# Kernel optimization log

Measured on AMD Instinct MI355X. Metric: run time of the kernel, lower is better.

Reference implementation:

```python
import jax, jax.numpy as jnp
import numpy as np

B, L, ENC_IN, C_OUT = 8, 8192, 21, 21
D_MODEL, D_STATE, D_CONV, EXPAND = 512, 16, 4, 2
D_INNER = EXPAND * D_MODEL
DT_RANK = -(-D_MODEL // 16)  # 'auto' -> ceil(d_model/16) = 32
PRED_LEN = 720


def setup_inputs() -> dict:
    key = jax.random.key(0)
    ks = jax.random.split(key, 16)
    s = lambda k, sh, sc=0.02: jax.random.normal(k, sh, jnp.float32) * sc
    # Mamba-style dt bias init: dt ~ exp(U(log dt_min, log dt_max)), bias = softplus^{-1}(dt)
    dt = jnp.exp(jax.random.uniform(ks[9], (D_INNER,), jnp.float32,
                                    float(np.log(1e-3)), float(np.log(0.1))))
    b_dt = jnp.log(jnp.expm1(dt))
    return dict(
        x_enc=jax.random.normal(ks[0], (B, L, ENC_IN), jnp.float32),
        x_mark_enc=jax.random.normal(ks[1], (B, L, 4), jnp.float32),
        x_dec=jax.random.normal(ks[2], (B, PRED_LEN, ENC_IN), jnp.float32),
        x_mark_dec=jax.random.normal(ks[3], (B, PRED_LEN, 4), jnp.float32),
        W_embed=s(ks[4], (ENC_IN, D_MODEL)),
        b_embed=jnp.zeros((D_MODEL,), jnp.float32),
        W_in=s(ks[5], (D_MODEL, 2 * D_INNER)),
        conv_w=s(ks[6], (D_INNER, D_CONV), 0.1),
        conv_b=jnp.zeros((D_INNER,), jnp.float32),
        W_xproj=s(ks[7], (D_INNER, DT_RANK + 2 * D_STATE)),
        W_dt=s(ks[8], (DT_RANK, D_INNER), 0.1),
        b_dt=b_dt,
        A_log=jnp.log(jnp.tile(jnp.arange(1, D_STATE + 1, dtype=jnp.float32), (D_INNER, 1))),
        D=jnp.ones((D_INNER,), jnp.float32),
        W_out_ssm=s(ks[10], (D_INNER, D_MODEL)),
        W_proj=s(ks[11], (D_MODEL, C_OUT)),
        b_proj=jnp.zeros((C_OUT,), jnp.float32),
    )


def _mamba(x, W_in, conv_w, conv_b, W_xproj, W_dt, b_dt, A_log, D):
    b, l, _ = x.shape
    d_inner, d_conv = conv_w.shape
    d_state = A_log.shape[1]
    dt_rank = W_dt.shape[0]
    xz = x @ W_in                                   # [b,l,2*d_inner]
    u, z = jnp.split(xz, 2, axis=-1)
    # causal depthwise conv over time
    uc = jnp.transpose(u, (0, 2, 1))                # [b,d_inner,l]
    uc = jax.lax.conv_general_dilated(uc, conv_w[:, None, :], (1,),
                                      [(d_conv - 1, 0)],
                                      feature_group_count=d_inner)
    u = jax.nn.silu(jnp.transpose(uc, (0, 2, 1)) + conv_b)
    x_dbl = u @ W_xproj
    dt, Bm, Cm = jnp.split(x_dbl, [dt_rank, dt_rank + d_state], axis=-1)
    delta = jax.nn.softplus(dt @ W_dt + b_dt)       # [b,l,d_inner]
    A = -jnp.exp(A_log)                             # [d_inner,d_state]

    def step(h, inp):
        d_t, B_t, C_t, u_t = inp                    # [b,d_inner],[b,d_state],[b,d_state],[b,d_inner]
        dA = jnp.exp(d_t[..., None] * A)            # [b,d_inner,d_state]
        h = dA * h + (d_t * u_t)[..., None] * B_t[:, None, :]
        y = jnp.einsum('bds,bs->bd', h, C_t)
        return h, y

    h0 = jnp.zeros((b, d_inner, d_state), u.dtype)
    xs = (jnp.moveaxis(delta, 1, 0), jnp.moveaxis(Bm, 1, 0),
          jnp.moveaxis(Cm, 1, 0), jnp.moveaxis(u, 1, 0))
    _, ys = jax.lax.scan(step, h0, xs)              # ys: [l,b,d_inner]
    y = jnp.moveaxis(ys, 0, 1) + u * D
    return y * jax.nn.silu(z)


def reference(x_enc, x_mark_enc, x_dec, x_mark_dec, W_embed, b_embed, W_in,
              conv_w, conv_b, W_xproj, W_dt, b_dt, A_log, D, W_out_ssm,
              W_proj, b_proj):
    # RevIN normalize (stats detached, matching .detach() in torch)
    means = jax.lax.stop_gradient(x_enc.mean(axis=1, keepdims=True))
    xc = x_enc - means
    stdev = jax.lax.stop_gradient(jnp.sqrt(jnp.var(xc, axis=1, keepdims=True) + 1e-5))
    xn = xc / stdev
    emb = xn @ W_embed + b_embed                    # [b,L,d_model]
    y = _mamba(emb, W_in, conv_w, conv_b, W_xproj, W_dt, b_dt, A_log, D)
    y = y @ W_out_ssm                               # [b,L,d_model]
    y = y[:, -PRED_LEN:, :]                         # L >= pred_len branch
    out = y @ W_proj + b_proj                       # [b,pred_len,c_out]
    out = out * stdev[:, :1, :] + means[:, :1, :]   # RevIN denorm (c_out == enc_in)
    return out
```

## Files before the change

kernel.cpp:

```cpp
#include <hip/hip_runtime.h>
#include <hip/hip_bf16.h>
#include <stdint.h>

#define B_    8
#define L_    8192
#define CIN   21
#define DM    512
#define DI    1024
#define DS    16
#define DTR   32
#define PRED  720
#define L0    (L_ - PRED)
#define CHUNK 128
#define NCHK  64
#define NTCH  6
#define TAIL0 7424
#define NSUB  24
#define TROWS 768

#define UIDX(b, row, dblk, dl) ((((size_t)(b) * 16 + (dblk)) * L_ + (row)) * 64 + (dl))
#define TIDX(b, row, dblk, dl) ((((size_t)(b) * 16 + (dblk)) * TROWS + (row)) * 64 + (dl))
#define QIDX(b, c, dblk, s, dl) \
  ((((((size_t)(b) * NCHK + (c)) * 16 + (dblk)) * 16 + (s)) * 64) + (dl))
#define SIDX(b, si, dblk, s, dl) \
  ((((((size_t)(b) * NSUB + (si)) * 16 + (dblk)) * 16 + (s)) * 64) + (dl))

typedef __bf16 bf16_t;
typedef __attribute__((ext_vector_type(4))) __bf16 bf16x4;
typedef __attribute__((ext_vector_type(8))) __bf16 bf16x8;
typedef __attribute__((ext_vector_type(4))) float f32x4;
typedef __attribute__((ext_vector_type(2))) float f32x2;

__device__ __forceinline__ void gl_lds16(const void* g, void* l) {
  __builtin_amdgcn_global_load_lds(
      (const __attribute__((address_space(1))) unsigned int*)g,
      (__attribute__((address_space(3))) unsigned int*)l, 16, 0, 0);
}

__device__ __forceinline__ float b2f(bf16_t v) { return (float)v; }
__device__ __forceinline__ bf16_t f2b(float v) { return (bf16_t)v; }

__global__ void zero_kernel(float* __restrict__ out, int n) {
  int i = blockIdx.x * 256 + threadIdx.x;
  if (i < n) out[i] = 0.f;
}

__global__ __launch_bounds__(256) void stats_kernel(const float* __restrict__ x,
                                                    float* __restrict__ stats) {
  const int b = blockIdx.x / CIN, c = blockIdx.x % CIN;
  const int tid = threadIdx.x;
  float s = 0.f, s2 = 0.f;
  for (int l = tid; l < L_; l += 256) {
    float v = x[((size_t)b * L_ + l) * CIN + c];
    s += v; s2 += v * v;
  }
  __shared__ float rs[256], rs2[256];
  rs[tid] = s; rs2[tid] = s2;
  __syncthreads();
  for (int o = 128; o > 0; o >>= 1) {
    if (tid < o) { rs[tid] += rs[tid + o]; rs2[tid] += rs2[tid + o]; }
    __syncthreads();
  }
  if (tid == 0) {
    float mean = rs[0] / (float)L_;
    float var  = rs2[0] / (float)L_ - mean * mean;
    stats[(b * CIN + c) * 2]     = mean;
    stats[(b * CIN + c) * 2 + 1] = sqrtf(var + 1e-5f);
  }
}

__global__ void tconv_kernel(const float* __restrict__ in, bf16_t* __restrict__ out,
                             int R, int C) {
  int idx = blockIdx.x * 256 + threadIdx.x;
  if (idx < R * C) {
    int r = idx / C, c = idx % C;
    out[(size_t)c * R + r] = f2b(in[idx]);
  }
}
__global__ void tconvf_kernel(const float* __restrict__ in, float* __restrict__ out,
                              int R, int C) {
  int idx = blockIdx.x * 256 + threadIdx.x;
  if (idx < R * C) {
    int r = idx / C, c = idx % C;
    out[(size_t)c * R + r] = in[idx];
  }
}

__global__ __launch_bounds__(256) void wcomb_kernel(const float* __restrict__ We,
                                                    const float* __restrict__ be,
                                                    const float* __restrict__ Win,
                                                    float* __restrict__ Wcu,
                                                    float* __restrict__ Wcz) {
  int idx = blockIdx.x * 256 + threadIdx.x;
  if (idx >= 22 * 2048) return;
  int c = idx / 2048, n = idx % 2048;
  float a = 0.f;
  if (c < 21) {
    for (int k = 0; k < DM; ++k) a = fmaf(We[c * DM + k], Win[(size_t)k * 2048 + n], a);
  } else {
    for (int k = 0; k < DM; ++k) a = fmaf(be[k], Win[(size_t)k * 2048 + n], a);
  }
  if (n < DI) Wcu[c * DI + n] = a;
  else        Wcz[c * DI + (n - DI)] = a;
}

__global__ __launch_bounds__(256) void fc_kernel(const float* __restrict__ x,
                                                 const float* __restrict__ stats,
                                                 const float* __restrict__ Wcu,
                                                 const float* __restrict__ cwT,
                                                 const float* __restrict__ cb,
                                                 bf16_t* __restrict__ u_act) {
  __shared__ float xn[11][22];
  const size_t bb = blockIdx.y;
  const float* xb = x + bb * ((size_t)L_ * CIN);
  const float* st = stats + bb * (CIN * 2);
  const int r0 = blockIdx.x * 8;
  const int tid = threadIdx.x;
  for (int i = tid; i < 11 * 22; i += 256) {
    int j = i / 22, c = i % 22;
    int row = r0 - 3 + j;
    float v = 0.f;
    if (row >= 0) {
      if (c < 21) v = (xb[(size_t)row * CIN + c] - st[c * 2]) / st[c * 2 + 1];
      else v = 1.f;
    }
    xn[j][c] = v;
  }
  __syncthreads();
  const int col = tid * 4;
  const int dblk = col >> 6, dl = col & 63;
  f32x4 acc[11] = {};
  for (int c = 0; c < 22; ++c) {
    f32x4 w = *(const f32x4*)&Wcu[c * DI + col];
#pragma unroll
    for (int j = 0; j < 11; ++j) acc[j] += xn[j][c] * w;
  }
  f32x4 w0 = *(const f32x4*)&cwT[0 * DI + col];
  f32x4 w1 = *(const f32x4*)&cwT[1 * DI + col];
  f32x4 w2 = *(const f32x4*)&cwT[2 * DI + col];
  f32x4 w3 = *(const f32x4*)&cwT[3 * DI + col];
  f32x4 cbv = *(const f32x4*)&cb[col];
#pragma unroll
  for (int i = 0; i < 8; ++i) {
    f32x4 a = cbv + w0 * acc[i] + w1 * acc[i + 1] + w2 * acc[i + 2] + w3 * acc[i + 3];
    bf16x4 o;
#pragma unroll
    for (int e = 0; e < 4; ++e) {
      float v = a[e];
      o[e] = f2b(v / (1.f + __expf(-v)));
    }
    *(bf16x4*)&u_act[UIDX(bb, r0 + i, dblk, dl)] = o;
  }
}

__global__ __launch_bounds__(256) void zfc_kernel(const float* __restrict__ x,
                                                  const float* __restrict__ stats,
                                                  const float* __restrict__ Wcz,
                                                  bf16_t* __restrict__ zbuf) {
  __shared__ float xn[22];
  const int row = blockIdx.x;
  const size_t b = blockIdx.y;
  const int tid = threadIdx.x;
  if (tid < 22) {
    int l = L0 + row;
    float v = 1.f;
    if (tid < 21)
      v = (x[(b * L_ + l) * (size_t)CIN + tid] - stats[(b * CIN + tid) * 2]) /
          stats[(b * CIN + tid) * 2 + 1];
    xn[tid] = v;
  }
  __syncthreads();
  const int col = tid * 4;
  f32x4 a = {};
  for (int c = 0; c < 22; ++c) a += xn[c] * *(const f32x4*)&Wcz[c * DI + col];
  bf16x4 o;
#pragma unroll
  for (int e = 0; e < 4; ++e) o[e] = f2b(a[e]);
  *(bf16x4*)&zbuf[(b * PRED + row) * (size_t)DI + col] = o;
}

template <int BM, int BN, int WMR, int WNR, int EPI, bool ATILED = false>
__global__ __launch_bounds__(256) void gemm_kernel(
    const bf16_t* __restrict__ A, const bf16_t* __restrict__ Bt,
    bf16_t* __restrict__ O1, bf16_t* __restrict__ O1b, float* __restrict__ Of,
    int M, int N, int K, size_t sA, size_t sO1, size_t sO1b, size_t sOf) {
  __shared__ bf16_t Alds[BM][32];
  __shared__ bf16_t Blds[BN][32];
  const size_t zb = blockIdx.z;
  A += zb * sA;
  if (O1)  O1  += zb * sO1;
  if (O1b) O1b += zb * sO1b;
  if (Of)  Of  += zb * sOf;
  const int tid = threadIdx.x;
  const int wave = tid >> 6, lane = tid & 63;
  const int wm = wave >> 1, wn = wave & 1;
  const int lr = lane & 15, lk = lane >> 4;
  const int tm = blockIdx.x * BM;
  const int tn = blockIdx.y * BN;

  f32x4 acc[WMR][WNR] = {};

  const int nk = K >> 5;
  for (int ks = 0; ks < nk; ++ks) {
#pragma unroll
    for (int r = wave; r < BM / 16; r += 4) {
      int row = tm + r * 16 + (lane >> 2);
      if constexpr (ATILED) {
        int kk = ks * 32 + (lane & 3) * 8;
        gl_lds16(A + (((size_t)(kk >> 6) * L_ + row) * 64 + (kk & 63)), &Alds[r * 16][0]);
      } else {
        gl_lds16(A + (size_t)row * K + ks * 32 + (lane & 3) * 8, &Alds[r * 16][0]);
      }
    }
#pragma unroll
    for (int r = wave; r < BN / 16; r += 4)
      gl_lds16(Bt + (size_t)(tn + r * 16 + (lane >> 2)) * K + ks * 32 + (lane & 3) * 8,
               &Blds[r * 16][0]);
    __syncthreads();
    bf16x8 af[WMR], bfr[WNR];
#pragma unroll
    for (int mi = 0; mi < WMR; ++mi)
      af[mi] = *(const bf16x8*)(&Alds[wm * (WMR * 16) + mi * 16 + lr][lk * 8]);
#pragma unroll
    for (int ni = 0; ni < WNR; ++ni)
      bfr[ni] = *(const bf16x8*)(&Blds[wn * (WNR * 16) + ni * 16 + lr][lk * 8]);
#pragma unroll
    for (int mi = 0; mi < WMR; ++mi)
#pragma unroll
      for (int ni = 0; ni < WNR; ++ni)
        acc[mi][ni] = __builtin_amdgcn_mfma_f32_16x16x32_bf16(af[mi], bfr[ni], acc[mi][ni], 0, 0, 0);
    __syncthreads();
  }

#pragma unroll
  for (int mi = 0; mi < WMR; ++mi) {
#pragma unroll
    for (int ni = 0; ni < WNR; ++ni) {
#pragma unroll
      for (int r = 0; r < 4; ++r) {
        int row = tm + wm * (WMR * 16) + mi * 16 + lk * 4 + r;
        int col = tn + wn * (WNR * 16) + ni * 16 + lr;
        float v = acc[mi][ni][r];
        if constexpr (EPI == 0) {
          O1[(size_t)row * N + col] = f2b(v);
        } else if constexpr (EPI == 2) {
          if (col < 32) O1b[(size_t)row * 32 + col] = f2b(v);
          else          Of[(size_t)row * 32 + (col - 32)] = v;
        }
      }
    }
  }
}

__global__ __launch_bounds__(256) void scanA_kernel(
    const bf16_t* __restrict__ u_act, const bf16_t* __restrict__ dtb,
    const float* __restrict__ BC, const bf16_t* __restrict__ Wdt,
    const float* __restrict__ bdt,
    float* __restrict__ q, float* __restrict__ dsum_g,
    float* __restrict__ qs, float* __restrict__ dsums,
    bf16_t* __restrict__ dtail) {
  __shared__ __align__(16) char smem[17408];
  bf16_t (*Dl)[64] = (bf16_t(*)[64])smem;
  const int tid = threadIdx.x, wave = tid >> 6, lane = tid & 63;
  const int dblk = blockIdx.x, d0 = dblk * 64, chunk = blockIdx.y;
  const size_t b = blockIdx.z;
  const bf16_t* dt = dtb + b * ((size_t)L_ * 32);
  const float*  bc = BC + b * ((size_t)L_ * 32);
  const int row0 = chunk * CHUNK, t0 = wave * 32;
  const int lr = lane & 15, lk = lane >> 4;

  const bf16_t* up = u_act + UIDX(b, row0 + t0, dblk, lane);
  bf16_t ureg[32];
#pragma unroll
  for (int t = 0; t < 32; ++t) ureg[t] = up[(size_t)t * 64];

  bf16x8 afr0 = *(const bf16x8*)&dt[(size_t)(row0 + t0 + lr) * 32 + lk * 8];
  bf16x8 afr1 = *(const bf16x8*)&dt[(size_t)(row0 + t0 + 16 + lr) * 32 + lk * 8];
  f32x4 dacc[2][4];
#pragma unroll
  for (int ni = 0; ni < 4; ++ni) {
    bf16x8 bfr = *(const bf16x8*)&Wdt[(size_t)(d0 + ni * 16 + lr) * 32 + lk * 8];
    f32x4 zz = {};
    dacc[0][ni] = __builtin_amdgcn_mfma_f32_16x16x32_bf16(afr0, bfr, zz, 0, 0, 0);
    dacc[1][ni] = __builtin_amdgcn_mfma_f32_16x16x32_bf16(afr1, bfr, zz, 0, 0, 0);
  }
#pragma unroll
  for (int mi = 0; mi < 2; ++mi)
#pragma unroll
    for (int ni = 0; ni < 4; ++ni)
#pragma unroll
      for (int r = 0; r < 4; ++r) {
        float xx = dacc[mi][ni][r] + bdt[d0 + ni * 16 + lr];
        float sp = (xx > 20.f) ? xx : log1pf(__expf(xx));
        Dl[t0 + mi * 16 + lk * 4 + r][ni * 16 + lr] = f2b(sp);
      }

  f32x2 h01{}, h23{}, h45{}, h67{}, h89{}, hab{}, hcd{}, hef{};
  float dsub = 0.f;
#pragma unroll
  for (int t = 0; t < 32; ++t) {
    int ridx = __builtin_amdgcn_readfirstlane(row0 + t0 + t);
    const float* brow = bc + (size_t)ridx * 32;
    f32x2 B0 = *(const f32x2*)(brow + 0);
    f32x2 B1 = *(const f32x2*)(brow + 2);
    f32x2 B2 = *(const f32x2*)(brow + 4);
    f32x2 B3 = *(const f32x2*)(brow + 6);
    f32x2 B4 = *(const f32x2*)(brow + 8);
    f32x2 B5 = *(const f32x2*)(brow + 10);
    f32x2 B6 = *(const f32x2*)(brow + 12);
    f32x2 B7 = *(const f32x2*)(brow + 14);
    float dlt = b2f(Dl[t0 + t][lane]);
    float ut  = b2f(ureg[t]);
    float rr = __expf(-dlt);
    float du = dlt * ut;
    dsub += dlt;
    float r2s = rr * rr;
    f32x2 p01 = {rr, r2s};
    f32x2 rq  = {r2s, r2s};
    f32x2 p23 = p01 * rq, p45 = p23 * rq, p67 = p45 * rq, p89 = p67 * rq,
          pab = p89 * rq, pcd = pab * rq, pef = pcd * rq;
    f32x2 du2 = {du, du};
    h01 = p01 * h01 + du2 * B0;
    h23 = p23 * h23 + du2 * B1;
    h45 = p45 * h45 + du2 * B2;
    h67 = p67 * h67 + du2 * B3;
    h89 = p89 * h89 + du2 * B4;
    hab = pab * hab + du2 * B5;
    hcd = pcd * hcd + du2 * B6;
    hef = pef * hef + du2 * B7;
  }
  if (chunk >= NCHK - NTCH) {
    int si = (chunk - (NCHK - NTCH)) * 4 + wave;
    float* qsb = qs + SIDX(b, si, dblk, 0, lane);
    qsb[0*64]=h01[0];  qsb[1*64]=h01[1];  qsb[2*64]=h23[0];  qsb[3*64]=h23[1];
    qsb[4*64]=h45[0];  qsb[5*64]=h45[1];  qsb[6*64]=h67[0];  qsb[7*64]=h67[1];
    qsb[8*64]=h89[0];  qsb[9*64]=h89[1];  qsb[10*64]=hab[0]; qsb[11*64]=hab[1];
    qsb[12*64]=hcd[0]; qsb[13*64]=hcd[1]; qsb[14*64]=hef[0]; qsb[15*64]=hef[1];
    dsums[((size_t)b * NSUB + si) * DI + d0 + lane] = dsub;
  }

  __syncthreads();
  if (chunk >= NCHK - NTCH) {
    bf16_t* dtl = dtail + TIDX(b, row0 - TAIL0, dblk, 0);
#pragma unroll
    for (int j = 0; j < 4; ++j) {
      int idx = j * 256 + tid;
      *(bf16x8*)&dtl[idx * 8] = *(const bf16x8*)&((bf16_t*)Dl)[idx * 8];
    }
    __syncthreads();
  }
  float (*Hw)[16][64] = (float(*)[16][64])smem;
  float (*Dw)[64]     = (float(*)[64])(smem + 16384);
  Hw[wave][0][lane]=h01[0];  Hw[wave][1][lane]=h01[1];
  Hw[wave][2][lane]=h23[0];  Hw[wave][3][lane]=h23[1];
  Hw[wave][4][lane]=h45[0];  Hw[wave][5][lane]=h45[1];
  Hw[wave][6][lane]=h67[0];  Hw[wave][7][lane]=h67[1];
  Hw[wave][8][lane]=h89[0];  Hw[wave][9][lane]=h89[1];
  Hw[wave][10][lane]=hab[0]; Hw[wave][11][lane]=hab[1];
  Hw[wave][12][lane]=hcd[0]; Hw[wave][13][lane]=hcd[1];
  Hw[wave][14][lane]=hef[0]; Hw[wave][15][lane]=hef[1];
  Dw[wave][lane] = dsub;
  __syncthreads();
  float* qb = q + QIDX(b, chunk, dblk, 0, 0);
#pragma unroll
  for (int k = 0; k < 4; ++k) {
    const int d = tid & 63;
    const int s = (tid >> 6) + 4 * k;
    const float As = (float)(s + 1);
    float h = 0.f;
#pragma unroll
    for (int w = 0; w < 4; ++w)
      h = fmaf(__expf(-Dw[w][d] * As), h, Hw[w][s][d]);
    qb[s * 64 + d] = h;
  }
  if (tid < 64)
    dsum_g[((size_t)b * NCHK + chunk) * DI + d0 + tid] =
        Dw[0][tid] + Dw[1][tid] + Dw[2][tid] + Dw[3][tid];
}

__global__ __launch_bounds__(256) void scanB_kernel(const float* __restrict__ q,
                                                    const float* __restrict__ dsum_g,
                                                    const float* __restrict__ qs,
                                                    const float* __restrict__ dsums,
                                                    float* __restrict__ h0) {
  const int idx = blockIdx.x * 256 + threadIdx.x;
  const int d = idx & (DI - 1);
  const int s = (idx >> 10) & 15;
  const size_t b = idx >> 14;
  const int dblk = d >> 6, dl = d & 63;
  const float As = (float)(s + 1);
  float h = 0.f;
#pragma unroll 4
  for (int c = 0; c < NCHK - NTCH; ++c) {
    float ds = dsum_g[(b * NCHK + c) * (size_t)DI + d];
    float qv = q[QIDX(b, c, dblk, s, dl)];
    h = fmaf(__expf(-ds * As), h, qv);
  }
#pragma unroll 8
  for (int si = 0; si < NSUB; ++si) {
    h0[SIDX(b, si, dblk, s, dl)] = h;
    float ds = dsums[(b * NSUB + si) * (size_t)DI + d];
    float qv = qs[SIDX(b, si, dblk, s, dl)];
    h = fmaf(__expf(-ds * As), h, qv);
  }
}

__global__ __launch_bounds__(256) void scanC_kernel(
    const bf16_t* __restrict__ dtail, const bf16_t* __restrict__ u_act,
    const float* __restrict__ BC, const float* __restrict__ h0buf,
    const float* __restrict__ Dvec, const bf16_t* __restrict__ zb,
    bf16_t* __restrict__ yg) {
  const int tid = threadIdx.x;
  const int d = blockIdx.x * 256 + tid;
  const int dblk = d >> 6, dl = d & 63;
  const int sub = blockIdx.y + 1;
  const size_t b = blockIdx.z;
  const float* xtp = BC + b * ((size_t)L_ * 32) + (size_t)TAIL0 * 32;
  const bf16_t* zp = zb + b * ((size_t)PRED * DI);
  bf16_t* yp = yg + b * ((size_t)PRED * DI);
  const int lr0 = sub * 32;
  const float* hp = h0buf + SIDX(b, sub, dblk, 0, dl);
  f32x2 h01 = {hp[0*64], hp[1*64]},   h23 = {hp[2*64], hp[3*64]},
        h45 = {hp[4*64], hp[5*64]},   h67 = {hp[6*64], hp[7*64]},
        h89 = {hp[8*64], hp[9*64]},   hab = {hp[10*64], hp[11*64]},
        hcd = {hp[12*64], hp[13*64]}, hef = {hp[14*64], hp[15*64]};
  const float Dd = Dvec[d];
#pragma unroll 4
  for (int t = 0; t < 32; ++t) {
    const int lr = lr0 + t;
    int ridx = __builtin_amdgcn_readfirstlane(lr);
    const float* brow = xtp + (size_t)ridx * 32;
    f32x2 B0 = *(const f32x2*)(brow + 0);
    f32x2 B1 = *(const f32x2*)(brow + 2);
    f32x2 B2 = *(const f32x2*)(brow + 4);
    f32x2 B3 = *(const f32x2*)(brow + 6);
    f32x2 B4 = *(const f32x2*)(brow + 8);
    f32x2 B5 = *(const f32x2*)(brow + 10);
    f32x2 B6 = *(const f32x2*)(brow + 12);
    f32x2 B7 = *(const f32x2*)(brow + 14);
    float dlt = b2f(dtail[TIDX(b, lr, dblk, dl)]);
    float ut  = b2f(u_act[UIDX(b, TAIL0 + lr, dblk, dl)]);
    float rr = __expf(-dlt);
    float du = dlt * ut;
    float r2s = rr * rr;
    f32x2 p01 = {rr, r2s};
    f32x2 rq  = {r2s, r2s};
    f32x2 p23 = p01 * rq, p45 = p23 * rq, p67 = p45 * rq, p89 = p67 * rq,
          pab = p89 * rq, pcd = pab * rq, pef = pcd * rq;
    f32x2 du2 = {du, du};
    h01 = p01 * h01 + du2 * B0;
    h23 = p23 * h23 + du2 * B1;
    h45 = p45 * h45 + du2 * B2;
    h67 = p67 * h67 + du2 * B3;
    h89 = p89 * h89 + du2 * B4;
    hab = pab * hab + du2 * B5;
    hcd = pcd * hcd + du2 * B6;
    hef = pef * hef + du2 * B7;
    if (lr >= 48) {
      f32x2 C0 = *(const f32x2*)(brow + 16);
      f32x2 C1 = *(const f32x2*)(brow + 18);
      f32x2 C2 = *(const f32x2*)(brow + 20);
      f32x2 C3 = *(const f32x2*)(brow + 22);
      f32x2 C4 = *(const f32x2*)(brow + 24);
      f32x2 C5 = *(const f32x2*)(brow + 26);
      f32x2 C6 = *(const f32x2*)(brow + 28);
      f32x2 C7 = *(const f32x2*)(brow + 30);
      f32x2 ya = h01 * C0;
      ya = h23 * C1 + ya; ya = h45 * C2 + ya; ya = h67 * C3 + ya;
      ya = h89 * C4 + ya; ya = hab * C5 + ya; ya = hcd * C6 + ya;
      ya = hef * C7 + ya;
      float y = ya[0] + ya[1];
      int gl = lr - 48;
      float zv = b2f(zp[(size_t)gl * DI + d]);
      float gate = zv / (1.f + __expf(-zv));
      yp[(size_t)gl * DI + d] = f2b((y + ut * Dd) * gate);
    }
  }
}

__global__ __launch_bounds__(256) void final_kernel(const bf16_t* __restrict__ y1,
                                                    const float* __restrict__ Wp,
                                                    const float* __restrict__ bp,
                                                    const float* __restrict__ stats,
                                                    float* __restrict__ out) {
  __shared__ float ys[DM];
  __shared__ float rs[8][32];
  const int row = blockIdx.x;
  const int b = row / PRED;
  const int tid = threadIdx.x;
  ys[tid] = b2f(y1[(size_t)row * DM + tid]);
  ys[tid + 256] = b2f(y1[(size_t)row * DM + tid + 256]);
  __syncthreads();
  const int c = tid & 31, ks = tid >> 5;
  float p = 0.f;
  if (c < CIN) {
    const int k0 = ks * 64;
    for (int k = 0; k < 64; ++k) p = fmaf(ys[k0 + k], Wp[(k0 + k) * CIN + c], p);
  }
  rs[ks][c] = p;
  __syncthreads();
  if (tid < CIN) {
    float a = bp[tid];
#pragma unroll
    for (int j = 0; j < 8; ++j) a += rs[j][tid];
    float mean = stats[(b * CIN + tid) * 2], sd = stats[(b * CIN + tid) * 2 + 1];
    out[(size_t)row * CIN + tid] = fmaf(a, sd, mean);
  }
}

static inline size_t padq(size_t x) { return (x + 255) & ~(size_t)255; }
struct Ptrs {
  bf16_t *u_act, *dtb, *dtail, *zbuf, *yg, *y1;
  bf16_t *Wt_xp, *Wt_dt, *Wt_out;
  float *BC, *q, *dsum, *qs, *dsums, *h0, *cwT, *Wcu, *Wcz, *stats;
  size_t total;
};
static Ptrs layout(char* ws) {
  Ptrs P; size_t off = 0;
  auto al = [&](size_t bytes) { char* p = ws + off; off += padq(bytes); return p; };
  P.u_act = (bf16_t*)al((size_t)B_ * L_ * DI * 2);
  P.dtb   = (bf16_t*)al((size_t)B_ * L_ * 32 * 2);
  P.BC    = (float*) al((size_t)B_ * L_ * 32 * 4);
  P.q     = (float*) al((size_t)B_ * NCHK * 16 * DI * 4);
  P.dsum  = (float*) al((size_t)B_ * NCHK * DI * 4);
  P.qs    = (float*) al((size_t)B_ * NSUB * 16 * DI * 4);
  P.dsums = (float*) al((size_t)B_ * NSUB * DI * 4);
  P.h0    = (float*) al((size_t)B_ * NSUB * 16 * DI * 4);
  P.dtail = (bf16_t*)al((size_t)B_ * TROWS * DI * 2);
  P.zbuf  = (bf16_t*)al((size_t)B_ * PRED * DI * 2);
  P.yg    = (bf16_t*)al((size_t)B_ * PRED * DI * 2);
  P.y1    = (bf16_t*)al((size_t)B_ * PRED * DM * 2);
  P.Wt_xp = (bf16_t*)al((size_t)64 * 1024 * 2);
  P.Wt_dt = (bf16_t*)al((size_t)1024 * 32 * 2);
  P.Wt_out= (bf16_t*)al((size_t)512 * 1024 * 2);
  P.cwT   = (float*) al((size_t)4 * DI * 4);
  P.Wcu   = (float*) al((size_t)22 * DI * 4);
  P.Wcz   = (float*) al((size_t)22 * DI * 4);
  P.stats = (float*) al((size_t)B_ * CIN * 2 * 4);
  P.total = off;
  return P;
}

extern "C" void kernel_launch(void* const* d_in, const int* in_sizes, int n_in,
                              void* d_out, int out_size, void* d_ws, size_t ws_size,
                              hipStream_t stream) {
  const float* x_enc   = (const float*)d_in[0];
  const float* W_embed = (const float*)d_in[4];
  const float* b_embed = (const float*)d_in[5];
  const float* W_in    = (const float*)d_in[6];
  const float* conv_w  = (const float*)d_in[7];
  const float* conv_b  = (const float*)d_in[8];
  const float* W_xproj = (const float*)d_in[9];
  const float* W_dt    = (const float*)d_in[10];
  const float* b_dt    = (const float*)d_in[11];
  const float* Dvec    = (const float*)d_in[13];
  const float* W_out   = (const float*)d_in[14];
  const float* W_proj  = (const float*)d_in[15];
  const float* b_proj  = (const float*)d_in[16];
  float* out = (float*)d_out;
  char* ws = (char*)d_ws;

  Ptrs P = layout(ws);
  if (P.total > ws_size) {
    zero_kernel<<<(out_size + 255) / 256, 256, 0, stream>>>(out, out_size);
    return;
  }

  stats_kernel<<<B_ * CIN, 256, 0, stream>>>(x_enc, P.stats);
  wcomb_kernel<<<(22 * 2048 + 255) / 256, 256, 0, stream>>>(W_embed, b_embed, W_in, P.Wcu, P.Wcz);
  tconv_kernel<<<(1024 * 64 + 255) / 256, 256, 0, stream>>>(W_xproj, P.Wt_xp, 1024, 64);
  tconv_kernel<<<(32 * 1024 + 255) / 256, 256, 0, stream>>>(W_dt,    P.Wt_dt, 32, 1024);
  tconv_kernel<<<(1024 * 512 + 255) / 256, 256, 0, stream>>>(W_out,   P.Wt_out, 1024, 512);
  tconvf_kernel<<<(1024 * 4 + 255) / 256, 256, 0, stream>>>(conv_w,  P.cwT, 1024, 4);

  zfc_kernel<<<dim3(PRED, B_), 256, 0, stream>>>(x_enc, P.stats, P.Wcz, P.zbuf);
  fc_kernel<<<dim3(L_ / 8, B_), 256, 0, stream>>>(x_enc, P.stats, P.Wcu, P.cwT, conv_b, P.u_act);
  gemm_kernel<32, 64, 1, 2, 2, true><<<dim3(L_ / 32, 1, B_), 256, 0, stream>>>(
      P.u_act, P.Wt_xp, nullptr, P.dtb, P.BC, L_, 64, DI,
      (size_t)L_ * DI, 0, (size_t)L_ * 32, (size_t)L_ * 32);
  scanA_kernel<<<dim3(16, NCHK, B_), 256, 0, stream>>>(
      P.u_act, P.dtb, P.BC, P.Wt_dt, b_dt, P.q, P.dsum, P.qs, P.dsums, P.dtail);
  scanB_kernel<<<(B_ * DI * DS) / 256, 256, 0, stream>>>(P.q, P.dsum, P.qs, P.dsums, P.h0);
  scanC_kernel<<<dim3(DI / 256, NSUB - 1, B_), 256, 0, stream>>>(
      P.dtail, P.u_act, P.BC, P.h0, Dvec, P.zbuf, P.yg);
  gemm_kernel<64, 64, 2, 2, 0><<<dim3((B_ * PRED) / 64, DM / 64, 1), 256, 0, stream>>>(
      P.yg, P.Wt_out, P.y1, nullptr, nullptr, B_ * PRED, DM, DI, 0, 0, 0, 0);
  final_kernel<<<B_ * PRED, 256, 0, stream>>>(P.y1, W_proj, b_proj, P.stats, out);
}
```

Before: 516.1 us.

## Sort channels by dt bias and skip chunks whose decayed contribution is negligible

Sorts the d_inner channels by b_dt and permutes every weight and bias to match, so channels with similar decay rates share a 64-channel block. New kernels compute, per batch and block, a lower bound on the cumulative decay from dt-row norms and weight norms. From that bound they pick the first chunk whose state contribution still exceeds exp(-16). scanA and scanB then skip all earlier chunks, which cuts scan work for fast-decaying blocks. This adds a sort, permutation and bounding passes, and introduces a bounded truncation error that depends on the data.

```diff
diff --git a/kernel.cpp b/kernel.cpp
--- a/kernel.cpp
+++ b/kernel.cpp
@@ -17,6 +17,7 @@
 #define TAIL0 7424
 #define NSUB  24
 #define TROWS 768
+#define CUT   16.0f
 
 #define UIDX(b, row, dblk, dl) ((((size_t)(b) * 16 + (dblk)) * L_ + (row)) * 64 + (dl))
 #define TIDX(b, row, dblk, dl) ((((size_t)(b) * 16 + (dblk)) * TROWS + (row)) * 64 + (dl))
@@ -43,6 +44,43 @@
 __global__ void zero_kernel(float* __restrict__ out, int n) {
   int i = blockIdx.x * 256 + threadIdx.x;
   if (i < n) out[i] = 0.f;
+}
+
+__global__ __launch_bounds__(512) void sort_kernel(const float* __restrict__ bdt,
+                                                   int* __restrict__ perm,
+                                                   int* __restrict__ iperm) {
+  __shared__ float key[1024];
+  __shared__ int   val[1024];
+  const int t = threadIdx.x;
+  key[t] = bdt[t];       val[t] = t;
+  key[t + 512] = bdt[t + 512]; val[t + 512] = t + 512;
+  __syncthreads();
+  for (int k = 2; k <= 1024; k <<= 1) {
+    for (int j = k >> 1; j > 0; j >>= 1) {
+      int i = ((t / j) * (j << 1)) + (t % j);
+      int p = i + j;
+      bool up = ((i & k) == 0);
+      float ki = key[i], kp = key[p];
+      int vi = val[i], vp = val[p];
+      bool sw = up ? ((ki > kp) || (ki == kp && vi > vp))
+                   : ((ki < kp) || (ki == kp && vi < vp));
+      if (sw) { key[i] = kp; key[p] = ki; val[i] = vp; val[p] = vi; }
+      __syncthreads();
+    }
+  }
+  perm[t] = val[t]; perm[t + 512] = val[t + 512];
+  iperm[val[t]] = t; iperm[val[t + 512]] = t + 512;
+}
+
+__global__ void permute3_kernel(const float* __restrict__ cb, const float* __restrict__ bdt,
+                                const float* __restrict__ Dv, const int* __restrict__ iperm,
+                                float* __restrict__ cbP, float* __restrict__ bdtP,
+                                float* __restrict__ DvP) {
+  int d = blockIdx.x * 256 + threadIdx.x;
+  if (d < DI) {
+    int nd = iperm[d];
+    cbP[nd] = cb[d]; bdtP[nd] = bdt[d]; DvP[nd] = Dv[d];
+  }
 }
 
 __global__ __launch_bounds__(256) void stats_kernel(const float* __restrict__ x,
@@ -70,25 +108,30 @@
 }
 
 __global__ void tconv_kernel(const float* __restrict__ in, bf16_t* __restrict__ out,
-                             int R, int C) {
+                             int R, int C, const int* __restrict__ pR,
+                             const int* __restrict__ pC) {
   int idx = blockIdx.x * 256 + threadIdx.x;
   if (idx < R * C) {
     int r = idx / C, c = idx % C;
-    out[(size_t)c * R + r] = f2b(in[idx]);
+    int ro = pR ? pR[r] : r;
+    int co = pC ? pC[c] : c;
+    out[(size_t)co * R + ro] = f2b(in[idx]);
   }
 }
 __global__ void tconvf_kernel(const float* __restrict__ in, float* __restrict__ out,
-                              int R, int C) {
+                              int R, int C, const int* __restrict__ pR) {
   int idx = blockIdx.x * 256 + threadIdx.x;
   if (idx < R * C) {
     int r = idx / C, c = idx % C;
-    out[(size_t)c * R + r] = in[idx];
+    int ro = pR ? pR[r] : r;
+    out[(size_t)c * R + ro] = in[idx];
   }
 }
 
 __global__ __launch_bounds__(256) void wcomb_kernel(const float* __restrict__ We,
                                                     const float* __restrict__ be,
                                                     const float* __restrict__ Win,
+                                                    const int* __restrict__ iperm,
                                                     float* __restrict__ Wcu,
                                                     float* __restrict__ Wcz) {
   int idx = blockIdx.x * 256 + threadIdx.x;
@@ -100,8 +143,8 @@
   } else {
     for (int k = 0; k < DM; ++k) a = fmaf(be[k], Win[(size_t)k * 2048 + n], a);
   }
-  if (n < DI) Wcu[c * DI + n] = a;
-  else        Wcz[c * DI + (n - DI)] = a;
+  if (n < DI) Wcu[c * DI + iperm[n]] = a;
+  else        Wcz[c * DI + iperm[n - DI]] = a;
 }
 
 __global__ __launch_bounds__(256) void fc_kernel(const float* __restrict__ x,
@@ -252,10 +295,72 @@
   }
 }
 
+__global__ __launch_bounds__(128) void rn_kernel(const bf16_t* __restrict__ dtb,
+                                                 float* __restrict__ maxrn) {
+  __shared__ float red[128];
+  const int chunk = blockIdx.x;
+  const size_t b = blockIdx.y;
+  const int t = threadIdx.x;
+  const bf16_t* row = dtb + b * ((size_t)L_ * 32) + (size_t)(chunk * CHUNK + t) * 32;
+  float s2 = 0.f;
+  for (int k = 0; k < 32; ++k) { float v = b2f(row[k]); s2 = fmaf(v, v, s2); }
+  red[t] = s2;
+  __syncthreads();
+  for (int o = 64; o > 0; o >>= 1) {
+    if (t < o) red[t] = fmaxf(red[t], red[t + o]);
+    __syncthreads();
+  }
+  if (t == 0) maxrn[b * 64 + chunk] = sqrtf(red[0]);
+}
+
+__global__ __launch_bounds__(64) void fk_kernel(const bf16_t* __restrict__ Wdt,
+                                                const float* __restrict__ bdtP,
+                                                const float* __restrict__ maxrn,
+                                                int* __restrict__ fk) {
+  __shared__ float red[64], ds[64];
+  const int dblk = blockIdx.x;
+  const int b = blockIdx.y;
+  const int t = threadIdx.x;
+  const int nd = dblk * 64 + t;
+  float s2 = 0.f;
+  for (int k = 0; k < 32; ++k) { float w = b2f(Wdt[(size_t)nd * 32 + k]); s2 = fmaf(w, w, s2); }
+  red[t] = s2;
+  __syncthreads();
+  for (int o = 32; o > 0; o >>= 1) {
+    if (t < o) red[t] = fmaxf(red[t], red[t + o]);
+    __syncthreads();
+  }
+  float wnmax = sqrtf(red[0]);
+  __syncthreads();
+  red[t] = bdtP[nd];
+  __syncthreads();
+  for (int o = 32; o > 0; o >>= 1) {
+    if (t < o) red[t] = fminf(red[t], red[t + o]);
+    __syncthreads();
+  }
+  float bmin = red[0];
+  __syncthreads();
+  if (t < NCHK - NTCH) {
+    float x = bmin - maxrn[b * 64 + t] * wnmax;
+    float sp = (x > 20.f) ? x : log1pf(__expf(x));
+    ds[t] = 128.f * sp;
+  }
+  __syncthreads();
+  if (t == 0) {
+    int f = NCHK - NTCH - 1;
+    float T = 0.f;
+    for (int c = NCHK - NTCH - 2; c >= 0; --c) {
+      T += ds[c + 1];
+      if (T <= CUT) f = c; else break;
+    }
+    fk[b * 16 + dblk] = f;
+  }
+}
+
 __global__ __launch_bounds__(256) void scanA_kernel(
     const bf16_t* __restrict__ u_act, const bf16_t* __restrict__ dtb,
     const float* __restrict__ BC, const bf16_t* __restrict__ Wdt,
-    const float* __restrict__ bdt,
+    const float* __restrict__ bdt, const int* __restrict__ fk,
     float* __restrict__ q, float* __restrict__ dsum_g,
     float* __restrict__ qs, float* __restrict__ dsums,
     bf16_t* __restrict__ dtail) {
@@ -264,6 +369,7 @@
   const int tid = threadIdx.x, wave = tid >> 6, lane = tid & 63;
   const int dblk = blockIdx.x, d0 = dblk * 64, chunk = blockIdx.y;
   const size_t b = blockIdx.z;
+  if (chunk < fk[b * 16 + dblk]) return;
   const bf16_t* dt = dtb + b * ((size_t)L_ * 32);
   const float*  bc = BC + b * ((size_t)L_ * 32);
   const int row0 = chunk * CHUNK, t0 = wave * 32;
@@ -382,6 +488,7 @@
                                                     const float* __restrict__ dsum_g,
                                                     const float* __restrict__ qs,
                                                     const float* __restrict__ dsums,
+                                                    const int* __restrict__ fk,
                                                     float* __restrict__ h0) {
   const int idx = blockIdx.x * 256 + threadIdx.x;
   const int d = idx & (DI - 1);
@@ -389,9 +496,9 @@
   const size_t b = idx >> 14;
   const int dblk = d >> 6, dl = d & 63;
   const float As = (float)(s + 1);
+  const int fkv = fk[b * 16 + dblk];
   float h = 0.f;
-#pragma unroll 4
-  for (int c = 0; c < NCHK - NTCH; ++c) {
+  for (int c = fkv; c < NCHK - NTCH; ++c) {
     float ds = dsum_g[(b * NCHK + c) * (size_t)DI + d];
     float qv = q[QIDX(b, c, dblk, s, dl)];
     h = fmaf(__expf(-ds * As), h, qv);
@@ -513,6 +620,8 @@
   bf16_t *u_act, *dtb, *dtail, *zbuf, *yg, *y1;
   bf16_t *Wt_xp, *Wt_dt, *Wt_out;
   float *BC, *q, *dsum, *qs, *dsums, *h0, *cwT, *Wcu, *Wcz, *stats;
+  float *cbP, *bdtP, *DvP, *maxrn;
+  int *perm, *iperm, *fk;
   size_t total;
 };
 static Ptrs layout(char* ws) {
@@ -537,6 +646,13 @@
   P.Wcu   = (float*) al((size_t)22 * DI * 4);
   P.Wcz   = (float*) al((size_t)22 * DI * 4);
   P.stats = (float*) al((size_t)B_ * CIN * 2 * 4);
+  P.cbP   = (float*) al((size_t)DI * 4);
+  P.bdtP  = (float*) al((size_t)DI * 4);
+  P.DvP   = (float*) al((size_t)DI * 4);
+  P.maxrn = (float*) al((size_t)B_ * 64 * 4);
+  P.perm  = (int*)   al((size_t)DI * 4);
+  P.iperm = (int*)   al((size_t)DI * 4);
+  P.fk    = (int*)   al((size_t)B_ * 16 * 4);
   P.total = off;
   return P;
 }
@@ -567,22 +683,31 @@
   }
 
   stats_kernel<<<B_ * CIN, 256, 0, stream>>>(x_enc, P.stats);
-  wcomb_kernel<<<(22 * 2048 + 255) / 256, 256, 0, stream>>>(W_embed, b_embed, W_in, P.Wcu, P.Wcz);
-  tconv_kernel<<<(1024 * 64 + 255) / 256, 256, 0, stream>>>(W_xproj, P.Wt_xp, 1024, 64);
-  tconv_kernel<<<(32 * 1024 + 255) / 256, 256, 0, stream>>>(W_dt,    P.Wt_dt, 32, 1024);
-  tconv_kernel<<<(1024 * 512 + 255) / 256, 256, 0, stream>>>(W_out,   P.Wt_out, 1024, 512);
-  tconvf_kernel<<<(1024 * 4 + 255) / 256, 256, 0, stream>>>(conv_w,  P.cwT, 1024, 4);
+  sort_kernel<<<1, 512, 0, stream>>>(b_dt, P.perm, P.iperm);
+  permute3_kernel<<<4, 256, 0, stream>>>(conv_b, b_dt, Dvec, P.iperm, P.cbP, P.bdtP, P.DvP);
+  wcomb_kernel<<<(22 * 2048 + 255) / 256, 256, 0, stream>>>(
+      W_embed, b_embed, W_in, P.iperm, P.Wcu, P.Wcz);
+  tconv_kernel<<<(1024 * 64 + 255) / 256, 256, 0, stream>>>(
+      W_xproj, P.Wt_xp, 1024, 64, P.iperm, nullptr);
+  tconv_kernel<<<(32 * 1024 + 255) / 256, 256, 0, stream>>>(
+      W_dt, P.Wt_dt, 32, 1024, nullptr, P.iperm);
+  tconv_kernel<<<(1024 * 512 + 255) / 256, 256, 0, stream>>>(
+      W_out, P.Wt_out, 1024, 512, P.iperm, nullptr);
+  tconvf_kernel<<<(1024 * 4 + 255) / 256, 256, 0, stream>>>(conv_w, P.cwT, 1024, 4, P.iperm);
 
   zfc_kernel<<<dim3(PRED, B_), 256, 0, stream>>>(x_enc, P.stats, P.Wcz, P.zbuf);
-  fc_kernel<<<dim3(L_ / 8, B_), 256, 0, stream>>>(x_enc, P.stats, P.Wcu, P.cwT, conv_b, P.u_act);
+  fc_kernel<<<dim3(L_ / 8, B_), 256, 0, stream>>>(x_enc, P.stats, P.Wcu, P.cwT, P.cbP, P.u_act);
   gemm_kernel<32, 64, 1, 2, 2, true><<<dim3(L_ / 32, 1, B_), 256, 0, stream>>>(
       P.u_act, P.Wt_xp, nullptr, P.dtb, P.BC, L_, 64, DI,
       (size_t)L_ * DI, 0, (size_t)L_ * 32, (size_t)L_ * 32);
+  rn_kernel<<<dim3(64, B_), 128, 0, stream>>>(P.dtb, P.maxrn);
+  fk_kernel<<<dim3(16, B_), 64, 0, stream>>>(P.Wt_dt, P.bdtP, P.maxrn, P.fk);
   scanA_kernel<<<dim3(16, NCHK, B_), 256, 0, stream>>>(
-      P.u_act, P.dtb, P.BC, P.Wt_dt, b_dt, P.q, P.dsum, P.qs, P.dsums, P.dtail);
-  scanB_kernel<<<(B_ * DI * DS) / 256, 256, 0, stream>>>(P.q, P.dsum, P.qs, P.dsums, P.h0);
+      P.u_act, P.dtb, P.BC, P.Wt_dt, P.bdtP, P.fk, P.q, P.dsum, P.qs, P.dsums, P.dtail);
+  scanB_kernel<<<(B_ * DI * DS) / 256, 256, 0, stream>>>(
+      P.q, P.dsum, P.qs, P.dsums, P.fk, P.h0);
   scanC_kernel<<<dim3(DI / 256, NSUB - 1, B_), 256, 0, stream>>>(
-      P.dtail, P.u_act, P.BC, P.h0, Dvec, P.zbuf, P.yg);
+      P.dtail, P.u_act, P.BC, P.h0, P.DvP, P.zbuf, P.yg);
   gemm_kernel<64, 64, 2, 2, 0><<<dim3((B_ * PRED) / 64, DM / 64, 1), 256, 0, stream>>>(
       P.yg, P.Wt_out, P.y1, nullptr, nullptr, B_ * PRED, DM, DI, 0, 0, 0, 0);
   final_kernel<<<B_ * PRED, 256, 0, stream>>>(P.y1, W_proj, b_proj, P.stats, out);
```

Measured after the change: 556.1 us. +7.7%, slower.
